# Optimization experiments

Hardware: AMD Instinct MI355X
Metric: run time of the kernel (lower is better)

The kernel has to match this reference:

```python
import jax, jax.numpy as jnp
import numpy as np

N_NODES = 100000
N_EDGES = 1600000
C_IN, C_HID, C_OUT = 64, 64, 32


def _gcn_conv(x, src, dst, ew, W, b, n_nodes):
    """PyG GCNConv: add self-loops (weight 1), symmetric normalization,
    out[dst] += norm * (x @ W)[src], plus bias. Dropout omitted (eval mode)."""
    h = x @ W  # [N, C_out_layer]
    loop = jnp.arange(n_nodes, dtype=src.dtype)
    src_a = jnp.concatenate([src, loop])
    dst_a = jnp.concatenate([dst, loop])
    ew_a = jnp.concatenate([ew, jnp.ones((n_nodes,), dtype=ew.dtype)])
    # degree over incoming (dst) side, weighted
    deg = jax.ops.segment_sum(ew_a, dst_a, num_segments=n_nodes)
    dinv = jnp.where(deg > 0, jax.lax.rsqrt(deg), 0.0)
    norm = dinv[src_a] * ew_a * dinv[dst_a]  # [E+N]
    msg = h[src_a] * norm[:, None]           # gather + scale: [E+N, C]
    out = jax.ops.segment_sum(msg, dst_a, num_segments=n_nodes)  # scatter-add
    return out + b


def setup_inputs() -> dict:
    key = jax.random.key(0)
    k1, k2, k3, k4, k5, k6, k7 = jax.random.split(key, 7)
    x = jax.random.normal(k1, (N_NODES, C_IN), dtype=jnp.float32)
    edge_index = jax.random.randint(k2, (2, N_EDGES), 0, N_NODES, dtype=jnp.int64)
    edge_attr = jax.random.uniform(k3, (N_EDGES,), dtype=jnp.float32)
    s1 = 1.0 / np.sqrt(C_IN)
    s2 = 1.0 / np.sqrt(C_HID)
    W1 = jax.random.uniform(k4, (C_IN, C_HID), jnp.float32, -s1, s1)
    b1 = jnp.zeros((C_HID,), dtype=jnp.float32)
    W2 = jax.random.uniform(k5, (C_HID, C_OUT), jnp.float32, -s2, s2)
    b2 = jnp.zeros((C_OUT,), dtype=jnp.float32)
    return {"x": x, "edge_index": edge_index, "edge_attr": edge_attr,
            "W1": W1, "b1": b1, "W2": W2, "b2": b2}


def reference(x, edge_index, edge_attr, W1, b1, W2, b2):
    n = x.shape[0]
    src, dst = edge_index[0], edge_index[1]
    h = _gcn_conv(x, src, dst, edge_attr, W1, b1, n)
    h = jax.nn.relu(h)  # dropout is identity in eval mode
    out = _gcn_conv(h, src, dst, edge_attr, W2, b2, n)
    return out
```

## Files before the change

kernel.cpp:

```cpp
#include <hip/hip_runtime.h>
#include <hip/hip_fp16.h>


#define TPB 256
#define TPB_P 512
#define TPB_S 1024
#define BSH2 8
#define BN2 256
#define NBC 512
#define BPAD 400
#define PCHUNK 4096
#define CAP2 5632
#define XSTR 68

typedef union { uint2 u; __half2 h[2]; } hpack;
typedef union { uint4 u; __half2 h[4]; } hpack8;

__device__ __forceinline__ int enc_w(float w) {
  unsigned b = __float_as_uint(w);
  return (int)(((b + 0x7FFFu + ((b >> 16) & 1u)) >> 16) & 0x7FFFu);
}
__device__ __forceinline__ float dec_w(int e) {
  return __uint_as_float(((unsigned)e >> 17) << 16);
}

__global__ __launch_bounds__(TPB_P) void k_fat(const int* __restrict__ di,
                                               int* __restrict__ bcnt,
                                               const float* __restrict__ x,
                                               const float* __restrict__ W1,
                                               __half* __restrict__ h1h,
                                               int e, int n, int gbp) {
  __shared__ union SM {
    int hcnt[NBC];
    float Wl[64 * 64];
  } sm;
  int t = threadIdx.x;
  if (blockIdx.x < (unsigned)gbp) {
    int lo = blockIdx.x * PCHUNK;
    int hi = lo + PCHUNK; if (hi > e) hi = e;
    sm.hcnt[t] = 0;
    __syncthreads();
    for (int i = lo + t; i < hi; i += TPB_P) atomicAdd(&sm.hcnt[di[i] >> BSH2], 1);
    __syncthreads();
    bcnt[t * BPAD + blockIdx.x] = sm.hcnt[t];
  } else {
    {
      const float4* W4 = (const float4*)W1;
      float4* Wl4 = (float4*)sm.Wl;
#pragma unroll
      for (int i = 0; i < 2; ++i) Wl4[t + TPB_P * i] = W4[t + TPB_P * i];
    }
    __syncthreads();
    int r = (blockIdx.x - gbp) * 32 + (t >> 4);
    if (r >= n) return;
    int c0 = (t & 15) << 2;
    const float4* xr = (const float4*)(x + (size_t)r * 64);
    float ax = 0.f, ay = 0.f, az = 0.f, aw = 0.f;
#pragma unroll
    for (int kk = 0; kk < 16; ++kk) {
      float4 xv = xr[kk];
      const float* w = &sm.Wl[(kk * 4) * 64 + c0];
      float4 w0 = *(const float4*)(w);
      float4 w1 = *(const float4*)(w + 64);
      float4 w2 = *(const float4*)(w + 128);
      float4 w3 = *(const float4*)(w + 192);
      ax += xv.x * w0.x + xv.y * w1.x + xv.z * w2.x + xv.w * w3.x;
      ay += xv.x * w0.y + xv.y * w1.y + xv.z * w2.y + xv.w * w3.y;
      az += xv.x * w0.z + xv.y * w1.z + xv.z * w2.z + xv.w * w3.z;
      aw += xv.x * w0.w + xv.y * w1.w + xv.z * w2.w + xv.w * w3.w;
    }
    hpack pk;
    pk.h[0] = __floats2half2_rn(ax, ay);
    pk.h[1] = __floats2half2_rn(az, aw);
    *(uint2*)(h1h + (size_t)r * 64 + c0) = pk.u;
  }
}

__global__ __launch_bounds__(64) void k_scan(const int* __restrict__ bcnt,
                                             int* __restrict__ bofs,
                                             int* __restrict__ bpos, int nblk) {
  int row = blockIdx.x, lane = threadIdx.x;
  const int* rp = bcnt + row * BPAD;
  int* op = bofs + row * BPAD;
  int base = row * CAP2;
  int carry = 0;
  for (int c0 = 0; c0 < nblk; c0 += 64) {
    int i = c0 + lane;
    int v = (i < nblk) ? rp[i] : 0;
    int orig = v;
#pragma unroll
    for (int off = 1; off < 64; off <<= 1) {
      int u = __shfl_up(v, off);
      if (lane >= off) v += u;
    }
    if (i < nblk) op[i] = base + carry + (v - orig);
    carry += __shfl(v, 63);
  }
  if (lane == 0) bpos[row] = carry;
}

__global__ __launch_bounds__(TPB_P) void k_scat(const int* __restrict__ si,
                                                const int* __restrict__ di,
                                                const float* __restrict__ ew,
                                                const int* __restrict__ bcnt,
                                                const int* __restrict__ bofs,
                                                int2* __restrict__ tin, int e) {
  __shared__ int lst0[NBC];
  __shared__ int lcur[NBC];
  __shared__ int hbase[NBC];
  __shared__ int wsum[8];
  __shared__ int2 se[PCHUNK];
  __shared__ unsigned short sbk[PCHUNK];
  int t = threadIdx.x, b = blockIdx.x;
  int lo = b * PCHUNK;
  int hi = lo + PCHUNK; if (hi > e) hi = e;
  int cn = hi - lo;
  int cb = bcnt[t * BPAD + b];
  hbase[t] = bofs[t * BPAD + b];
  lcur[t] = 0;
  int lane = t & 63, wid = t >> 6;
  int v = cb;
#pragma unroll
  for (int off = 1; off < 64; off <<= 1) {
    int u = __shfl_up(v, off);
    if (lane >= off) v += u;
  }
  if (lane == 63) wsum[wid] = v;
  __syncthreads();
  if (t < 64) {
    int s = (t < 8) ? wsum[t] : 0;
#pragma unroll
    for (int off = 1; off < 8; off <<= 1) {
      int u = __shfl_up(s, off);
      if (t >= off) s += u;
    }
    if (t < 8) wsum[t] = s;
  }
  __syncthreads();
  int incl = v + (wid ? wsum[wid - 1] : 0);
  lst0[t] = incl - cb;
  __syncthreads();
  for (int i = lo + t; i < hi; i += TPB_P) {
    int d = di[i];
    int bk = d >> BSH2;
    int loc = atomicAdd(&lcur[bk], 1);
    int p = lst0[bk] + loc;
    se[p] = make_int2(si[i] | ((d & (BN2 - 1)) << 17), __float_as_int(ew[i]));
    sbk[p] = (unsigned short)bk;
  }
  __syncthreads();
  for (int p = t; p < cn; p += TPB_P) {
    int bk = sbk[p];
    tin[hbase[bk] + (p - lst0[bk])] = se[p];
  }
}

__global__ __launch_bounds__(TPB_S) void k_sortb(const int2* __restrict__ tin,
                                                 const int* __restrict__ bpos,
                                                 int* __restrict__ colpk,
                                                 int2* __restrict__ rowseg,
                                                 float* __restrict__ dinv, int n) {
  __shared__ int cnt[BN2];
  __shared__ float degw[BN2];
  __shared__ int cur[BN2];
  __shared__ int ls[BN2];
  __shared__ int2 se[PCHUNK];
  int b = blockIdx.x, t = threadIdx.x;
  if (t < BN2) { cnt[t] = 0; degw[t] = 1.0f; }
  __syncthreads();
  int jb = b * CAP2, je = jb + bpos[b];
  for (int j = jb + t; j < je; j += TPB_S) {
    int2 p = tin[j];
    int o = j - jb;
    if (o < PCHUNK) se[o] = p;
    int dl = p.x >> 17;
    atomicAdd(&cnt[dl], 1);
    atomicAdd(&degw[dl], __int_as_float(p.y));
  }
  __syncthreads();
  int c = (t < BN2) ? cnt[t] : 0;
  int c4 = (c + 3) & ~3;
  if (t < BN2) ls[t] = c4;
  __syncthreads();
  for (int off = 1; off < BN2; off <<= 1) {
    int u = (t >= off && t < BN2) ? ls[t - off] : 0;
    __syncthreads();
    if (t < BN2) ls[t] += u;
    __syncthreads();
  }
  int base = b << BSH2;
  if (t < BN2) {
    int start = jb + ls[t] - c4;
    cur[t] = start;
    int node = base + t;
    if (node < n) {
      rowseg[node] = make_int2(start, start + c4);
      dinv[node] = rsqrtf(degw[t]);
    }
    for (int i = c; i < c4; ++i) colpk[start + i] = 0;
  }
  __syncthreads();
  for (int j = jb + t; j < je; j += TPB_S) {
    int o = j - jb;
    int2 p = (o < PCHUNK) ? se[o] : tin[j];
    int dl = p.x >> 17;
    int pos = atomicAdd(&cur[dl], 1);
    colpk[pos] = (p.x & 0x1FFFF) | (enc_w(__int_as_float(p.y)) << 17);
  }
}

__global__ __launch_bounds__(TPB) void k_gfuse(const __half* __restrict__ g1h,
                                               const int* __restrict__ colpk,
                                               const int2* __restrict__ rowseg,
                                               const float* __restrict__ dinv,
                                               const float* __restrict__ W2,
                                               const float* __restrict__ b1,
                                               __half* __restrict__ g2h, int n) {
  __shared__ float W2l[64 * 32];
  __shared__ float b1l[64];
  __shared__ float x2l[32 * XSTR];
  int t = threadIdx.x;
  {
    const float4* W4 = (const float4*)W2;
    float4* Wl4 = (float4*)W2l;
#pragma unroll
    for (int i = 0; i < 2; ++i) Wl4[t + TPB * i] = W4[t + TPB * i];
    if (t < 64) b1l[t] = b1[t];
  }
  __syncthreads();
  int node = t >> 3;
  int r = blockIdx.x * 32 + node;
  int c0 = (t & 7) << 3;
  bool valid = (r < n);
  float a[8];
  float dv = 0.f;
  if (valid) {
    dv = dinv[r];
    hpack8 s; s.u = *(const uint4*)(g1h + (size_t)r * 64 + c0);
#pragma unroll
    for (int k = 0; k < 4; ++k) {
      float2 f = __half22float2(s.h[k]);
      a[2 * k] = dv * f.x; a[2 * k + 1] = dv * f.y;
    }
    int2 seg = rowseg[r];
    int j = seg.x;
    for (; j + 7 < seg.y; j += 8) {
      int4 qa = *(const int4*)(colpk + j);
      int4 qb = *(const int4*)(colpk + j + 4);
      int s0 = qa.x & 0x1FFFF, s1 = qa.y & 0x1FFFF, s2 = qa.z & 0x1FFFF, s3 = qa.w & 0x1FFFF;
      int s4 = qb.x & 0x1FFFF, s5 = qb.y & 0x1FFFF, s6 = qb.z & 0x1FFFF, s7 = qb.w & 0x1FFFF;
      hpack8 u0; u0.u = *(const uint4*)(g1h + (size_t)s0 * 64 + c0);
      hpack8 u1; u1.u = *(const uint4*)(g1h + (size_t)s1 * 64 + c0);
      hpack8 u2; u2.u = *(const uint4*)(g1h + (size_t)s2 * 64 + c0);
      hpack8 u3; u3.u = *(const uint4*)(g1h + (size_t)s3 * 64 + c0);
      hpack8 u4; u4.u = *(const uint4*)(g1h + (size_t)s4 * 64 + c0);
      hpack8 u5; u5.u = *(const uint4*)(g1h + (size_t)s5 * 64 + c0);
      hpack8 u6; u6.u = *(const uint4*)(g1h + (size_t)s6 * 64 + c0);
      hpack8 u7; u7.u = *(const uint4*)(g1h + (size_t)s7 * 64 + c0);
      float w0 = dec_w(qa.x) * dinv[s0], w1 = dec_w(qa.y) * dinv[s1];
      float w2 = dec_w(qa.z) * dinv[s2], w3 = dec_w(qa.w) * dinv[s3];
      float w4 = dec_w(qb.x) * dinv[s4], w5 = dec_w(qb.y) * dinv[s5];
      float w6 = dec_w(qb.z) * dinv[s6], w7 = dec_w(qb.w) * dinv[s7];
#pragma unroll
      for (int k = 0; k < 4; ++k) {
        float2 f;
        f = __half22float2(u0.h[k]); a[2*k] += w0 * f.x; a[2*k+1] += w0 * f.y;
        f = __half22float2(u1.h[k]); a[2*k] += w1 * f.x; a[2*k+1] += w1 * f.y;
        f = __half22float2(u2.h[k]); a[2*k] += w2 * f.x; a[2*k+1] += w2 * f.y;
        f = __half22float2(u3.h[k]); a[2*k] += w3 * f.x; a[2*k+1] += w3 * f.y;
        f = __half22float2(u4.h[k]); a[2*k] += w4 * f.x; a[2*k+1] += w4 * f.y;
        f = __half22float2(u5.h[k]); a[2*k] += w5 * f.x; a[2*k+1] += w5 * f.y;
        f = __half22float2(u6.h[k]); a[2*k] += w6 * f.x; a[2*k+1] += w6 * f.y;
        f = __half22float2(u7.h[k]); a[2*k] += w7 * f.x; a[2*k+1] += w7 * f.y;
      }
    }
    if (j < seg.y) {
      int4 qa = *(const int4*)(colpk + j);
      int s0 = qa.x & 0x1FFFF, s1 = qa.y & 0x1FFFF, s2 = qa.z & 0x1FFFF, s3 = qa.w & 0x1FFFF;
      hpack8 u0; u0.u = *(const uint4*)(g1h + (size_t)s0 * 64 + c0);
      hpack8 u1; u1.u = *(const uint4*)(g1h + (size_t)s1 * 64 + c0);
      hpack8 u2; u2.u = *(const uint4*)(g1h + (size_t)s2 * 64 + c0);
      hpack8 u3; u3.u = *(const uint4*)(g1h + (size_t)s3 * 64 + c0);
      float w0 = dec_w(qa.x) * dinv[s0], w1 = dec_w(qa.y) * dinv[s1];
      float w2 = dec_w(qa.z) * dinv[s2], w3 = dec_w(qa.w) * dinv[s3];
#pragma unroll
      for (int k = 0; k < 4; ++k) {
        float2 f;
        f = __half22float2(u0.h[k]); a[2*k] += w0 * f.x; a[2*k+1] += w0 * f.y;
        f = __half22float2(u1.h[k]); a[2*k] += w1 * f.x; a[2*k+1] += w1 * f.y;
        f = __half22float2(u2.h[k]); a[2*k] += w2 * f.x; a[2*k+1] += w2 * f.y;
        f = __half22float2(u3.h[k]); a[2*k] += w3 * f.x; a[2*k+1] += w3 * f.y;
      }
    }
    float* xp = x2l + node * XSTR + c0;
#pragma unroll
    for (int k = 0; k < 8; k += 4) {
      float4 v = {fmaxf(dv * a[k + 0] + b1l[c0 + k + 0], 0.f),
                  fmaxf(dv * a[k + 1] + b1l[c0 + k + 1], 0.f),
                  fmaxf(dv * a[k + 2] + b1l[c0 + k + 2], 0.f),
                  fmaxf(dv * a[k + 3] + b1l[c0 + k + 3], 0.f)};
      *(float4*)(xp + k) = v;
    }
  }
  __syncthreads();
  if (!valid) return;
  int oc = (t & 7) << 2;
  const float* xr = x2l + node * XSTR;
  float ax = 0.f, ay = 0.f, az = 0.f, aw = 0.f;
#pragma unroll
  for (int kk = 0; kk < 16; ++kk) {
    float4 xv = *(const float4*)(xr + 4 * kk);
    const float* w = &W2l[(kk * 4) * 32 + oc];
    float4 w0 = *(const float4*)(w);
    float4 w1 = *(const float4*)(w + 32);
    float4 w2 = *(const float4*)(w + 64);
    float4 w3 = *(const float4*)(w + 96);
    ax += xv.x * w0.x + xv.y * w1.x + xv.z * w2.x + xv.w * w3.x;
    ay += xv.x * w0.y + xv.y * w1.y + xv.z * w2.y + xv.w * w3.y;
    az += xv.x * w0.z + xv.y * w1.z + xv.z * w2.z + xv.w * w3.z;
    aw += xv.x * w0.w + xv.y * w1.w + xv.z * w2.w + xv.w * w3.w;
  }
  hpack pk;
  pk.h[0] = __floats2half2_rn(ax, ay);
  pk.h[1] = __floats2half2_rn(az, aw);
  *(uint2*)(g2h + (size_t)r * 32 + oc) = pk.u;
}

__global__ __launch_bounds__(TPB) void k_gather32(const __half* __restrict__ g2h,
                                                  const int* __restrict__ colpk,
                                                  const int2* __restrict__ rowseg,
                                                  const float* __restrict__ dinv,
                                                  const float* __restrict__ b2,
                                                  float* __restrict__ out, int n) {
  int t = threadIdx.x;
  int r = blockIdx.x * 64 + (t >> 2);
  if (r >= n) return;
  int c0 = (t & 3) << 3;
  float dv = dinv[r];
  float a[8];
  {
    hpack8 s; s.u = *(const uint4*)(g2h + (size_t)r * 32 + c0);
#pragma unroll
    for (int k = 0; k < 4; ++k) {
      float2 f = __half22float2(s.h[k]);
      a[2 * k] = dv * f.x; a[2 * k + 1] = dv * f.y;
    }
  }
  int2 seg = rowseg[r];
  int j = seg.x;
  for (; j + 7 < seg.y; j += 8) {
    int4 qa = *(const int4*)(colpk + j);
    int4 qb = *(const int4*)(colpk + j + 4);
    int s0 = qa.x & 0x1FFFF, s1 = qa.y & 0x1FFFF, s2 = qa.z & 0x1FFFF, s3 = qa.w & 0x1FFFF;
    int s4 = qb.x & 0x1FFFF, s5 = qb.y & 0x1FFFF, s6 = qb.z & 0x1FFFF, s7 = qb.w & 0x1FFFF;
    hpack8 u0; u0.u = *(const uint4*)(g2h + (size_t)s0 * 32 + c0);
    hpack8 u1; u1.u = *(const uint4*)(g2h + (size_t)s1 * 32 + c0);
    hpack8 u2; u2.u = *(const uint4*)(g2h + (size_t)s2 * 32 + c0);
    hpack8 u3; u3.u = *(const uint4*)(g2h + (size_t)s3 * 32 + c0);
    hpack8 u4; u4.u = *(const uint4*)(g2h + (size_t)s4 * 32 + c0);
    hpack8 u5; u5.u = *(const uint4*)(g2h + (size_t)s5 * 32 + c0);
    hpack8 u6; u6.u = *(const uint4*)(g2h + (size_t)s6 * 32 + c0);
    hpack8 u7; u7.u = *(const uint4*)(g2h + (size_t)s7 * 32 + c0);
    float w0 = dec_w(qa.x) * dinv[s0], w1 = dec_w(qa.y) * dinv[s1];
    float w2 = dec_w(qa.z) * dinv[s2], w3 = dec_w(qa.w) * dinv[s3];
    float w4 = dec_w(qb.x) * dinv[s4], w5 = dec_w(qb.y) * dinv[s5];
    float w6 = dec_w(qb.z) * dinv[s6], w7 = dec_w(qb.w) * dinv[s7];
#pragma unroll
    for (int k = 0; k < 4; ++k) {
      float2 f;
      f = __half22float2(u0.h[k]); a[2*k] += w0 * f.x; a[2*k+1] += w0 * f.y;
      f = __half22float2(u1.h[k]); a[2*k] += w1 * f.x; a[2*k+1] += w1 * f.y;
      f = __half22float2(u2.h[k]); a[2*k] += w2 * f.x; a[2*k+1] += w2 * f.y;
      f = __half22float2(u3.h[k]); a[2*k] += w3 * f.x; a[2*k+1] += w3 * f.y;
      f = __half22float2(u4.h[k]); a[2*k] += w4 * f.x; a[2*k+1] += w4 * f.y;
      f = __half22float2(u5.h[k]); a[2*k] += w5 * f.x; a[2*k+1] += w5 * f.y;
      f = __half22float2(u6.h[k]); a[2*k] += w6 * f.x; a[2*k+1] += w6 * f.y;
      f = __half22float2(u7.h[k]); a[2*k] += w7 * f.x; a[2*k+1] += w7 * f.y;
    }
  }
  if (j < seg.y) {
    int4 qa = *(const int4*)(colpk + j);
    int s0 = qa.x & 0x1FFFF, s1 = qa.y & 0x1FFFF, s2 = qa.z & 0x1FFFF, s3 = qa.w & 0x1FFFF;
    hpack8 u0; u0.u = *(const uint4*)(g2h + (size_t)s0 * 32 + c0);
    hpack8 u1; u1.u = *(const uint4*)(g2h + (size_t)s1 * 32 + c0);
    hpack8 u2; u2.u = *(const uint4*)(g2h + (size_t)s2 * 32 + c0);
    hpack8 u3; u3.u = *(const uint4*)(g2h + (size_t)s3 * 32 + c0);
    float w0 = dec_w(qa.x) * dinv[s0], w1 = dec_w(qa.y) * dinv[s1];
    float w2 = dec_w(qa.z) * dinv[s2], w3 = dec_w(qa.w) * dinv[s3];
#pragma unroll
    for (int k = 0; k < 4; ++k) {
      float2 f;
      f = __half22float2(u0.h[k]); a[2*k] += w0 * f.x; a[2*k+1] += w0 * f.y;
      f = __half22float2(u1.h[k]); a[2*k] += w1 * f.x; a[2*k+1] += w1 * f.y;
      f = __half22float2(u2.h[k]); a[2*k] += w2 * f.x; a[2*k+1] += w2 * f.y;
      f = __half22float2(u3.h[k]); a[2*k] += w3 * f.x; a[2*k+1] += w3 * f.y;
    }
  }
  const float4* b24 = (const float4*)(b2 + c0);
  float4 bb0 = b24[0], bb1 = b24[1];
  float* op = out + (size_t)r * 32 + c0;
  *(float4*)(op)     = make_float4(dv * a[0] + bb0.x, dv * a[1] + bb0.y,
                                   dv * a[2] + bb0.z, dv * a[3] + bb0.w);
  *(float4*)(op + 4) = make_float4(dv * a[4] + bb1.x, dv * a[5] + bb1.y,
                                   dv * a[6] + bb1.z, dv * a[7] + bb1.w);
}

extern "C" void kernel_launch(void* const* d_in, const int* in_sizes, int n_in,
                              void* d_out, int out_size, void* d_ws, size_t ws_size,
                              hipStream_t stream) {
  const float* x  = (const float*)d_in[0];
  const int* ei   = (const int*)d_in[1];
  const float* ew = (const float*)d_in[2];
  const float* W1 = (const float*)d_in[3];
  const float* b1 = (const float*)d_in[4];
  const float* W2 = (const float*)d_in[5];
  const float* b2 = (const float*)d_in[6];
  float* out = (float*)d_out;

  const int n = in_sizes[0] / 64;
  const int e = in_sizes[1] / 2;
  const int* si = ei;
  const int* di = ei + e;
  const int NBc = (n + BN2 - 1) >> BSH2;

  float* ws = (float*)d_ws;
  const size_t NP = 100352;
  const size_t SLOTS = (size_t)NBc * CAP2;
  float*  dinv   = ws;
  __half* g1h    = (__half*)(ws + NP);
  int2*   rowseg = (int2*)(ws + NP + (size_t)n * 32);
  int*    bpos   = (int*)(rowseg + NP);
  int*    bcnt   = bpos + 1024;
  int*    bofs   = bcnt + NBC * BPAD;
  int*    colpk  = bofs + NBC * BPAD;
  int2*   tin    = (int2*)(colpk + SLOTS);
  __half* g2h    = (__half*)(tin + SLOTS);

  int gb_part = (e + PCHUNK - 1) / PCHUNK;
  int gb_g1 = (n + 31) / 32;
  int gb_gf = (n + 31) / 32;
  int gb_g32 = (n + 63) / 64;

  k_fat<<<gb_part + gb_g1, TPB_P, 0, stream>>>(di, bcnt, x, W1, g1h, e, n, gb_part);
  k_scan<<<NBC, 64, 0, stream>>>(bcnt, bofs, bpos, gb_part);
  k_scat<<<gb_part, TPB_P, 0, stream>>>(si, di, ew, bcnt, bofs, tin, e);
  k_sortb<<<NBc, TPB_S, 0, stream>>>(tin, bpos, colpk, rowseg, dinv, n);
  k_gfuse<<<gb_gf, TPB, 0, stream>>>(g1h, colpk, rowseg, dinv, W2, b1, g2h, n);
  k_gather32<<<gb_g32, TPB, 0, stream>>>(g2h, colpk, rowseg, dinv, b2, out, n);
}
```

Baseline: 205.8 us.

## Sort nodes by degree within buckets to balance gather workloads

k_sortb now builds a per-bucket permutation that groups each 256-node bucket by padded in-degree through a counting sort over degree bins. The two gather kernels read their node id through this permutation, so neighbouring threads in a wavefront process rows of similar length and spend less time idle on divergence. The cost is an extra perm array, an indirect load per row, and scattered row accesses in place of contiguous ones for g1h, rowseg, dinv and the outputs. Slots past n in the last bucket are padded so that r >= n is skipped.

After: 223.6 us. 1.09x slower.

```diff
diff --git a/kernel.cpp b/kernel.cpp
--- a/kernel.cpp
+++ b/kernel.cpp
@@ -159,11 +159,14 @@
                                                  const int* __restrict__ bpos,
                                                  int* __restrict__ colpk,
                                                  int2* __restrict__ rowseg,
-                                                 float* __restrict__ dinv, int n) {
+                                                 float* __restrict__ dinv,
+                                                 int* __restrict__ perm, int n) {
   __shared__ int cnt[BN2];
   __shared__ float degw[BN2];
   __shared__ int cur[BN2];
   __shared__ int ls[BN2];
+  __shared__ int dh[BN2];
+  __shared__ int dcur[BN2];
   __shared__ int2 se[PCHUNK];
   int b = blockIdx.x, t = threadIdx.x;
   if (t < BN2) { cnt[t] = 0; degw[t] = 1.0f; }
@@ -199,6 +202,26 @@
     }
     for (int i = c; i < c4; ++i) colpk[start + i] = 0;
   }
+  if (t < BN2) { dh[t] = 0; dcur[t] = 0; }
+  __syncthreads();
+  int bin = 0;
+  if (t < BN2) {
+    bin = c4 >> 2; if (bin > BN2 - 1) bin = BN2 - 1;
+    atomicAdd(&dh[bin], 1);
+  }
+  __syncthreads();
+  if (t < BN2) ls[t] = dh[t];
+  __syncthreads();
+  for (int off = 1; off < BN2; off <<= 1) {
+    int u = (t >= off && t < BN2) ? ls[t - off] : 0;
+    __syncthreads();
+    if (t < BN2) ls[t] += u;
+    __syncthreads();
+  }
+  if (t < BN2) {
+    int rank = atomicAdd(&dcur[bin], 1);
+    perm[base + (ls[bin] - dh[bin]) + rank] = base + t;
+  }
   __syncthreads();
   for (int j = jb + t; j < je; j += TPB_S) {
     int o = j - jb;
@@ -215,6 +238,7 @@
                                                const float* __restrict__ dinv,
                                                const float* __restrict__ W2,
                                                const float* __restrict__ b1,
+                                               const int* __restrict__ perm,
                                                __half* __restrict__ g2h, int n) {
   __shared__ float W2l[64 * 32];
   __shared__ float b1l[64];
@@ -229,7 +253,8 @@
   }
   __syncthreads();
   int node = t >> 3;
-  int r = blockIdx.x * 32 + node;
+  int slot = blockIdx.x * 32 + node;
+  int r = perm[slot];
   int c0 = (t & 7) << 3;
   bool valid = (r < n);
   float a[8];
@@ -331,9 +356,11 @@
                                                   const int2* __restrict__ rowseg,
                                                   const float* __restrict__ dinv,
                                                   const float* __restrict__ b2,
+                                                  const int* __restrict__ perm,
                                                   float* __restrict__ out, int n) {
   int t = threadIdx.x;
-  int r = blockIdx.x * 64 + (t >> 2);
+  int slot = blockIdx.x * 64 + (t >> 2);
+  int r = perm[slot];
   if (r >= n) return;
   int c0 = (t & 3) << 3;
   float dv = dinv[r];
@@ -422,6 +449,7 @@
   const int* si = ei;
   const int* di = ei + e;
   const int NBc = (n + BN2 - 1) >> BSH2;
+  const int NS = NBc << BSH2;
 
   float* ws = (float*)d_ws;
   const size_t NP = 100352;
@@ -432,19 +460,20 @@
   int*    bpos   = (int*)(rowseg + NP);
   int*    bcnt   = bpos + 1024;
   int*    bofs   = bcnt + NBC * BPAD;
-  int*    colpk  = bofs + NBC * BPAD;
+  int*    perm   = bofs + NBC * BPAD;
+  int*    colpk  = perm + NP;
   int2*   tin    = (int2*)(colpk + SLOTS);
   __half* g2h    = (__half*)(tin + SLOTS);
 
   int gb_part = (e + PCHUNK - 1) / PCHUNK;
   int gb_g1 = (n + 31) / 32;
-  int gb_gf = (n + 31) / 32;
-  int gb_g32 = (n + 63) / 64;
+  int gb_gf = NS / 32;
+  int gb_g32 = NS / 64;
 
   k_fat<<<gb_part + gb_g1, TPB_P, 0, stream>>>(di, bcnt, x, W1, g1h, e, n, gb_part);
   k_scan<<<NBC, 64, 0, stream>>>(bcnt, bofs, bpos, gb_part);
   k_scat<<<gb_part, TPB_P, 0, stream>>>(si, di, ew, bcnt, bofs, tin, e);
-  k_sortb<<<NBc, TPB_S, 0, stream>>>(tin, bpos, colpk, rowseg, dinv, n);
-  k_gfuse<<<gb_gf, TPB, 0, stream>>>(g1h, colpk, rowseg, dinv, W2, b1, g2h, n);
-  k_gather32<<<gb_g32, TPB, 0, stream>>>(g2h, colpk, rowseg, dinv, b2, out, n);
-}
+  k_sortb<<<NBc, TPB_S, 0, stream>>>(tin, bpos, colpk, rowseg, dinv, perm, n);
+  k_gfuse<<<gb_gf, TPB, 0, stream>>>(g1h, colpk, rowseg, dinv, W2, b1, perm, g2h, n);
+  k_gather32<<<gb_g32, TPB, 0, stream>>>(g2h, colpk, rowseg, dinv, b2, perm, out, n);
+}
```
